# Optimization experiments

Hardware: AMD Instinct MI355X
Metric: run time of the kernel (lower is better)

## Reference

```python
import jax, jax.numpy as jnp
import numpy as np

STRIDES = (8, 16, 32, 64, 128)
IMG = 1024
RANGES = ((-1.0, 64.0), (64.0, 128.0), (128.0, 256.0), (256.0, 512.0), (512.0, 1e8))
NUM_CLASSES = 15
TOPK = 15
BG_LABEL = 15  # hardcoded in the torch source
G = 32


def _grid():
    pts, rr, spp = [], [], []
    for s, (lo, hi) in zip(STRIDES, RANGES):
        n = IMG // s
        ys, xs = np.meshgrid(np.arange(n), np.arange(n), indexing='ij')
        p = np.stack([xs.ravel() * s + s / 2.0, ys.ravel() * s + s / 2.0], axis=-1)
        pts.append(p)
        rr.append(np.tile(np.array([lo, hi]), (n * n, 1)))
        spp.append(np.full(n * n, s, np.float32))
    return (np.concatenate(pts).astype(np.float32),
            np.concatenate(rr).astype(np.float32),
            np.concatenate(spp).astype(np.float32))


def setup_inputs():
    key = jax.random.key(0)
    k = jax.random.split(key, 7)
    pts, rr, spp = _grid()
    N = pts.shape[0]
    ctr = jax.random.uniform(k[0], (G, 2), minval=64.0, maxval=IMG - 64.0)
    wh = jax.random.uniform(k[1], (G, 2), minval=16.0, maxval=256.0)
    ang = jax.random.uniform(k[2], (G, 1), minval=-jnp.pi / 2, maxval=jnp.pi / 2)
    gt_bboxes = jnp.concatenate([ctr, wh, ang], -1)
    gt_labels = jax.random.randint(k[3], (G,), 0, NUM_CLASSES)
    dist = jax.random.uniform(k[4], (N, 4), minval=0.1, maxval=8.0)
    angp = jax.random.normal(k[5], (N, 1)) * 0.3
    bbox_preds = jnp.concatenate([dist, angp], -1)
    probs = jax.random.normal(k[6], (N, NUM_CLASSES))
    return {"points": jnp.asarray(pts), "regress_ranges": jnp.asarray(rr),
            "stride_pp": jnp.asarray(spp), "gt_bboxes": gt_bboxes,
            "gt_labels": gt_labels, "bbox_preds": bbox_preds, "probs": probs}


def _cross(a, b):
    return a[..., 0] * b[..., 1] - a[..., 1] * b[..., 0]


def _corners(boxes):
    # [...,5] (cx,cy,w,h,a) -> [...,4,2]
    c, s = jnp.cos(boxes[..., 4]), jnp.sin(boxes[..., 4])
    w2, h2 = boxes[..., 2] / 2, boxes[..., 3] / 2
    dx = jnp.stack([w2, w2, -w2, -w2], -1)
    dy = jnp.stack([-h2, h2, h2, -h2], -1)
    x = boxes[..., 0:1] + dx * c[..., None] - dy * s[..., None]
    y = boxes[..., 1:2] + dx * s[..., None] + dy * c[..., None]
    return jnp.stack([x, y], -1)


def _in_obb(pts, boxes, eps=1e-6):
    r = pts - boxes[..., :2]
    c, s = jnp.cos(boxes[..., 4]), jnp.sin(boxes[..., 4])
    x = r[..., 0] * c + r[..., 1] * s
    y = -r[..., 0] * s + r[..., 1] * c
    return (jnp.abs(x) <= boxes[..., 2] / 2 + eps) & (jnp.abs(y) <= boxes[..., 3] / 2 + eps)


def pairwise_riou(b1, b2):
    # exact rotated-box IoU, b1 [N,5] x b2 [G,5] -> [N,G]
    N, Gn = b1.shape[0], b2.shape[0]
    c1, c2 = _corners(b1), _corners(b2)
    p = c1[:, None, :, None, :]
    d1 = (jnp.roll(c1, -1, 1) - c1)[:, None, :, None, :]
    q = c2[None, :, None, :, :]
    d2 = (jnp.roll(c2, -1, 1) - c2)[None, :, None, :, :]
    den = _cross(d1, d2)                     # [N,G,4,4]
    safe = jnp.where(jnp.abs(den) > 1e-10, den, 1.0)
    qp = q - p
    t = _cross(qp, d2) / safe
    u = _cross(qp, d1) / safe
    ok = (jnp.abs(den) > 1e-10) & (t >= 0) & (t <= 1) & (u >= 0) & (u <= 1)
    inter_pts = p + t[..., None] * d1        # [N,G,4,4,2]
    pts_a = inter_pts.reshape(N, Gn, 16, 2)
    ok_a = ok.reshape(N, Gn, 16)
    v1 = jnp.broadcast_to(c1[:, None], (N, Gn, 4, 2))
    ok1 = _in_obb(c1[:, None, :, :], b2[None, :, None, :])
    v2 = jnp.broadcast_to(c2[None, :], (N, Gn, 4, 2))
    ok2 = _in_obb(c2[None, :, :, :], b1[:, None, None, :])
    pts = jnp.concatenate([pts_a, v1, v2], 2)    # [N,G,24,2]
    okm = jnp.concatenate([ok_a, ok1, ok2], 2)
    cnt = okm.sum(-1)
    ctr = jnp.sum(pts * okm[..., None], 2) / jnp.maximum(cnt, 1)[..., None]
    pts = jnp.where(okm[..., None], pts, ctr[..., None, :])
    ang = jnp.where(okm, jnp.arctan2(pts[..., 1] - ctr[..., None, 1],
                                     pts[..., 0] - ctr[..., None, 0]), 1e9)
    order = jnp.argsort(ang, -1)
    pts_s = jnp.take_along_axis(pts, order[..., None], 2)
    m = jnp.maximum(cnt, 1)[..., None]
    nxt = (jnp.arange(24) + 1)[None, None] % m   # triangle-fan wrap over valid pts
    pts_n = jnp.take_along_axis(pts_s, nxt[..., None], 2)
    va = pts_s - ctr[..., None, :]
    vb = pts_n - ctr[..., None, :]
    inter = 0.5 * jnp.abs(jnp.sum(_cross(va, vb), -1))
    a1 = (b1[:, 2] * b1[:, 3])[:, None]
    a2 = (b2[:, 2] * b2[:, 3])[None]
    return inter / jnp.maximum(a1 + a2 - inter, 1e-8)


def _decode(points, preds):
    # DistanceAnglePointCoder.decode (le90)
    dist, angle = preds[:, :4], preds[:, 4]
    c, s = jnp.cos(angle), jnp.sin(angle)
    wh = dist[:, :2] + dist[:, 2:]
    ot = (dist[:, 2:] - dist[:, :2]) / 2
    ox = c * ot[:, 0] - s * ot[:, 1]
    oy = s * ot[:, 0] + c * ot[:, 1]
    ctr = points + jnp.stack([ox, oy], -1)
    a = (angle + jnp.pi / 2) % jnp.pi - jnp.pi / 2
    return jnp.concatenate([ctr, wh, a[:, None]], -1)


def _assign(points, regress_ranges, stride_pp, gt_bboxes, bbox_preds, probs, gt_labels):
    N = points.shape[0]
    Gn = gt_bboxes.shape[0]
    gt_ctr, gt_wh, gt_angle = gt_bboxes[:, :2], gt_bboxes[:, 2:4], gt_bboxes[:, 4]
    c, s = jnp.cos(gt_angle), jnp.sin(gt_angle)
    off = points[:, None, :] - gt_ctr[None]               # [N,G,2]
    ox = off[..., 0] * c + off[..., 1] * s                # rot_matrix [[c,s],[-s,c]] @ off
    oy = -off[..., 0] * s + off[..., 1] * c
    w, h = gt_wh[:, 0], gt_wh[:, 1]
    bbox_targets = jnp.stack([w / 2 + ox, h / 2 + oy, w / 2 - ox, h / 2 - oy], -1)  # l,t,r,b
    inside_gt = bbox_targets.min(-1) > 0
    centerness = jnp.maximum(1 - jnp.sqrt(((2 * ox / w) ** 2 + (2 * oy / h) ** 2 + 1e-8) / 2), 0.0)
    max_rd = bbox_targets.max(-1)
    inside_rr = (max_rd >= regress_ranges[:, None, 0]) & (max_rd <= regress_ranges[:, None, 1])
    ctr_r = 1.5 * stride_pp[:, None]
    inside_gt = inside_gt & (jnp.abs(ox) < ctr_r) & (jnp.abs(oy) < ctr_r)
    valid = inside_gt & inside_rr                          # [N,G]
    scaled = jnp.concatenate([bbox_preds[:, :4] * stride_pp[:, None], bbox_preds[:, 4:]], -1)
    det_rbboxes = _decode(points, scaled)
    iou = pairwise_riou(det_rbboxes, gt_bboxes)            # [N,G]
    det_probs = jax.nn.softmax(probs, -1)
    cost = (0.2 * centerness + 0.2 * iou + 0.6 * det_probs[:, gt_labels]) * valid
    vals, idxs = jax.lax.top_k(cost.T, TOPK)               # per-GT topk, [G,k]
    topk_mask = jnp.zeros((N, Gn), bool).at[idxs.T, jnp.arange(Gn)[None, :]].set(vals.T != 0)
    areas = (w * h)[None] * valid * topk_mask
    max_area = areas.max(1)
    inds = jnp.argmax(areas, 1)
    labels = jnp.where(max_area == 0, BG_LABEL, gt_labels[inds])
    # rematch GTs that got no candidate point (bincount logic)
    matched = (max_area != 0).astype(jnp.int32)
    counts = jnp.zeros(Gn, jnp.int32).at[inds].add(matched)
    anchor = jnp.argmax(centerness, 0)                     # best-centerness point per GT
    upd = jnp.where(counts == 0, anchor, N)                # N is OOB -> dropped
    inds = inds.at[upd].set(jnp.arange(Gn), mode='drop')
    labels = labels.at[upd].set(gt_labels, mode='drop')
    bt = jnp.take_along_axis(bbox_targets, inds[:, None, None], 1)[:, 0] / stride_pp[:, None]
    at = gt_angle[inds][:, None]
    return labels, bt, at


def reference(points, regress_ranges, stride_pp, gt_bboxes, gt_labels, bbox_preds, probs):
    return _assign(points, regress_ranges, stride_pp, gt_bboxes, bbox_preds, probs, gt_labels)
```

## Files before the change

kernel.cpp:

```cpp
#include <hip/hip_runtime.h>
#include <math.h>

#define NC 15
#define TOPKK 15
#define BG_F 15.0f
#define MAXC 256

__device__ __forceinline__ float obb_iou_reg(
    float cx1, float cy1, float w1, float h1, float a1,
    float cx2, float cy2, float w2, float h2, float a2) {
  const float dxs[4] = {0.5f, 0.5f, -0.5f, -0.5f};
  const float dys[4] = {-0.5f, 0.5f, 0.5f, -0.5f};
  float c1 = cosf(a1), s1 = sinf(a1), c2 = cosf(a2), s2 = sinf(a2);
  float ax[4], ay[4], bx[4], by[4];
#pragma unroll
  for (int k = 0; k < 4; k++) {
    float dx = dxs[k] * w1, dy = dys[k] * h1;
    ax[k] = cx1 + dx * c1 - dy * s1;
    ay[k] = cy1 + dx * s1 + dy * c1;
    dx = dxs[k] * w2; dy = dys[k] * h2;
    bx[k] = cx2 + dx * c2 - dy * s2;
    by[k] = cy2 + dx * s2 + dy * c2;
  }
  float qx[24], qy[24];
#pragma unroll
  for (int k = 0; k < 24; k++) { qx[k] = 0.f; qy[k] = 0.f; }
  unsigned valid = 0u;
#pragma unroll
  for (int e1 = 0; e1 < 4; e1++) {
    float d1x = ax[(e1 + 1) & 3] - ax[e1], d1y = ay[(e1 + 1) & 3] - ay[e1];
#pragma unroll
    for (int e2 = 0; e2 < 4; e2++) {
      float d2x = bx[(e2 + 1) & 3] - bx[e2], d2y = by[(e2 + 1) & 3] - by[e2];
      float den = d1x * d2y - d1y * d2x;
      float qpx = bx[e2] - ax[e1], qpy = by[e2] - ay[e1];
      float t = (qpx * d2y - qpy * d2x) / den;
      float u = (qpx * d1y - qpy * d1x) / den;
      bool ok = (fabsf(den) > 1e-10f) &&
                (t >= 0.f) && (t <= 1.f) && (u >= 0.f) && (u <= 1.f);
      if (ok) {
        qx[e1 * 4 + e2] = ax[e1] + t * d1x;
        qy[e1 * 4 + e2] = ay[e1] + t * d1y;
        valid |= (1u << (e1 * 4 + e2));
      }
    }
  }
  const float eps = 1e-6f;
#pragma unroll
  for (int k = 0; k < 4; k++) {
    float rx = ax[k] - cx2, ry = ay[k] - cy2;
    float x = rx * c2 + ry * s2, y = -rx * s2 + ry * c2;
    if (fabsf(x) <= w2 * 0.5f + eps && fabsf(y) <= h2 * 0.5f + eps) {
      qx[16 + k] = ax[k]; qy[16 + k] = ay[k];
      valid |= (1u << (16 + k));
    }
  }
#pragma unroll
  for (int k = 0; k < 4; k++) {
    float rx = bx[k] - cx1, ry = by[k] - cy1;
    float x = rx * c1 + ry * s1, y = -rx * s1 + ry * c1;
    if (fabsf(x) <= w1 * 0.5f + eps && fabsf(y) <= h1 * 0.5f + eps) {
      qx[20 + k] = bx[k]; qy[20 + k] = by[k];
      valid |= (1u << (20 + k));
    }
  }
  int cnt = __popc(valid);
  float inter = 0.f;
  if (cnt > 0) {
    float sx = 0.f, sy = 0.f;
#pragma unroll
    for (int k = 0; k < 24; k++) {
      bool v = (valid >> k) & 1u;
      sx += v ? qx[k] : 0.f;
      sy += v ? qy[k] : 0.f;
    }
    float ccx = sx / (float)cnt, ccy = sy / (float)cnt;
    float ang[24];
#pragma unroll
    for (int k = 0; k < 24; k++) {
      float a = atan2f(qy[k] - ccy, qx[k] - ccx);
      ang[k] = ((valid >> k) & 1u) ? a : 1e9f;
    }
    unsigned used = ~valid;
    float area2 = 0.f;
    float prevx = 0.f, prevy = 0.f, firstx = 0.f, firsty = 0.f;
    for (int s = 0; s < cnt; s++) {
      float ba = 1e30f, bxv = 0.f, byv = 0.f;
      int bk = 0;
#pragma unroll
      for (int k = 0; k < 24; k++) {
        bool avail = !((used >> k) & 1u);
        bool better = avail && (ang[k] < ba);
        if (better) { ba = ang[k]; bxv = qx[k]; byv = qy[k]; bk = k; }
      }
      used |= (1u << bk);
      float vx = bxv - ccx, vy = byv - ccy;
      if (s == 0) { firstx = vx; firsty = vy; }
      else { area2 += prevx * vy - prevy * vx; }
      prevx = vx; prevy = vy;
    }
    area2 += prevx * firsty - prevy * firstx;
    inter = 0.5f * fabsf(area2);
  }
  float areaA = w1 * h1, areaB = w2 * h2;
  return inter / fmaxf(areaA + areaB - inter, 1e-8f);
}

__global__ void k_scan(const float* __restrict__ pts,
                       const float* __restrict__ rr,
                       const float* __restrict__ spp,
                       const float* __restrict__ gtb,
                       int* __restrict__ cand_cnt,
                       int* __restrict__ cand_i,
                       unsigned long long* __restrict__ blk_cent,
                       unsigned long long* __restrict__ point_key,
                       int N, int G) {
  int blk = blockIdx.x;
  int g = blk % G, chunk = blk / G;
  int i = chunk * 256 + threadIdx.x;
  if (g == 0 && i < N) point_key[i] = 0ull;
  float gx = gtb[g * 5 + 0], gy = gtb[g * 5 + 1];
  float gw = gtb[g * 5 + 2], gh = gtb[g * 5 + 3], ga = gtb[g * 5 + 4];
  float cg = cosf(ga), sg = sinf(ga);
  float inv_gw = 2.f / gw, inv_gh = 2.f / gh;
  float hw = gw * 0.5f, hh = gh * 0.5f;

  unsigned long long key = 0ull;
  bool valid = false;
  if (i < N) {
    float2 p = ((const float2*)pts)[i];
    float px = p.x - gx, py = p.y - gy;
    float ox = px * cg + py * sg, oy = -px * sg + py * cg;
    float nx = ox * inv_gw, ny = oy * inv_gh;
    float ctn = fmaxf(1.f - sqrtf((nx * nx + ny * ny + 1e-8f) * 0.5f), 0.f);
    key = ((unsigned long long)__float_as_uint(ctn) << 32) |
          (unsigned long long)(0xFFFFFFFFu - (unsigned)i);
    float l = hw + ox, tt = hh + oy, r = hw - ox, b = hh - oy;
    float minb = fminf(fminf(l, tt), fminf(r, b));
    float maxb = fmaxf(fmaxf(l, tt), fmaxf(r, b));
    float cr = 1.5f * spp[i];
    float2 rv = ((const float2*)rr)[i];
    valid = (minb > 0.f) && (fabsf(ox) < cr) && (fabsf(oy) < cr) &&
            (maxb >= rv.x) && (maxb <= rv.y);
  }
  unsigned long long best = key;
#pragma unroll
  for (int o = 32; o > 0; o >>= 1) {
    unsigned long long other = __shfl_xor(best, o, 64);
    if (other > best) best = other;
  }
  __shared__ unsigned long long swin[4];
  int lane = threadIdx.x & 63, wid = threadIdx.x >> 6;
  if (lane == 0) swin[wid] = best;
  __syncthreads();
  if (threadIdx.x == 0) {
    unsigned long long m = swin[0];
#pragma unroll
    for (int q = 1; q < 4; q++) if (swin[q] > m) m = swin[q];
    blk_cent[blk] = m;
  }
  unsigned long long ball = __ballot(valid);
  if (ball) {
    int leader = __ffsll(ball) - 1;
    int base = 0;
    if (lane == leader) base = atomicAdd(&cand_cnt[g], __popcll(ball));
    base = __shfl(base, leader, 64);
    if (valid) {
      int slot = base + __popcll(ball & ((1ull << lane) - 1ull));
      if (slot < MAXC) cand_i[g * MAXC + slot] = i;
    }
  }
}

__global__ void k_all(const float* __restrict__ pts,
                      const float* __restrict__ spp,
                      const float* __restrict__ gtb,
                      const int* __restrict__ gtl,
                      const float* __restrict__ preds,
                      const float* __restrict__ probs,
                      const int* __restrict__ cand_cnt,
                      const int* __restrict__ cand_i,
                      const unsigned long long* __restrict__ blk_cent,
                      unsigned long long* __restrict__ cent_key,
                      unsigned long long* __restrict__ point_key,
                      int G, int CH) {
  int g = blockIdx.x;
  int tid = threadIdx.x;
  int lane = tid & 63, wid = tid >> 6;
  float gx = gtb[g * 5 + 0], gy = gtb[g * 5 + 1];
  float gw = gtb[g * 5 + 2], gh = gtb[g * 5 + 3], ga = gtb[g * 5 + 4];
  float cg = cosf(ga), sg = sinf(ga);
  float inv_gw = 2.f / gw, inv_gh = 2.f / gh;
  __shared__ unsigned long long swin[4];

  unsigned long long best = 0ull;
  for (int c = tid; c < CH; c += 256) {
    unsigned long long e = blk_cent[(size_t)c * G + g];
    if (e > best) best = e;
  }
#pragma unroll
  for (int o = 32; o > 0; o >>= 1) {
    unsigned long long other = __shfl_xor(best, o, 64);
    if (other > best) best = other;
  }
  if (lane == 0) swin[wid] = best;
  __syncthreads();
  if (tid == 0) {
    unsigned long long m = swin[0];
#pragma unroll
    for (int q = 1; q < 4; q++) if (swin[q] > m) m = swin[q];
    cent_key[g] = m;
  }
  __syncthreads();

  int cnt = cand_cnt[g];
  if (cnt > MAXC) cnt = MAXC;

  unsigned long long key = 0ull;
  if (tid < cnt) {
    int i = cand_i[g * MAXC + tid];
    float ptx = pts[i * 2 + 0], pty = pts[i * 2 + 1];
    float px = ptx - gx, py = pty - gy;
    float ox = px * cg + py * sg, oy = -px * sg + py * cg;
    float nx = ox * inv_gw, ny = oy * inv_gh;
    float ctn = fmaxf(1.f - sqrtf((nx * nx + ny * ny + 1e-8f) * 0.5f), 0.f);

    float pv[NC];
    float m = -1e30f;
#pragma unroll
    for (int k = 0; k < NC; k++) { pv[k] = probs[i * NC + k]; m = fmaxf(m, pv[k]); }
    float ss = 0.f;
#pragma unroll
    for (int k = 0; k < NC; k++) { pv[k] = expf(pv[k] - m); ss += pv[k]; }
    float prob = pv[gtl[g]] / ss;

    float st = spp[i];
    float d0 = preds[i * 5 + 0] * st, d1 = preds[i * 5 + 1] * st;
    float d2 = preds[i * 5 + 2] * st, d3 = preds[i * 5 + 3] * st;
    float angp = preds[i * 5 + 4];
    float c = cosf(angp), s = sinf(angp);
    float w = d0 + d2, h = d1 + d3;
    float otx = (d2 - d0) * 0.5f, oty = (d3 - d1) * 0.5f;
    float dox = c * otx - s * oty, doy = s * otx + c * oty;
    const float PI = 3.14159265358979323846f;
    float a = fmodf(angp + PI * 0.5f, PI);
    if (a < 0.f) a += PI;
    a -= PI * 0.5f;

    float iou = obb_iou_reg(ptx + dox, pty + doy, w, h, a,
                            gx, gy, gw, gh, ga);
    float cval = 0.2f * ctn + 0.2f * iou + 0.6f * prob;
    key = ((unsigned long long)__float_as_uint(cval) << 32) |
          (unsigned long long)(0xFFFFFFFFu - (unsigned)i);
  }

  float area = gw * gh;
  unsigned long long area_key =
      (((unsigned long long)__float_as_uint(area)) << 32) |
      (unsigned long long)(unsigned)(G - 1 - g);
  int rounds = cnt < TOPKK ? cnt : TOPKK;
  for (int r = 0; r < rounds; r++) {
    unsigned long long k2 = key;
#pragma unroll
    for (int o = 32; o > 0; o >>= 1) {
      unsigned long long other = __shfl_xor(k2, o, 64);
      if (other > k2) k2 = other;
    }
    if (lane == 0) swin[wid] = k2;
    __syncthreads();
    unsigned long long w = swin[0];
#pragma unroll
    for (int q = 1; q < 4; q++) if (swin[q] > w) w = swin[q];
    __syncthreads();
    if (w == 0ull) break;
    if (key == w) key = 0ull;
    if (tid == 0) {
      unsigned iwin = 0xFFFFFFFFu - (unsigned)(w & 0xFFFFFFFFull);
      atomicMax(&point_key[iwin], area_key);
    }
  }
}

__global__ void k_assign(const unsigned long long* __restrict__ point_key,
                         const float* __restrict__ pts,
                         const float* __restrict__ spp,
                         const float* __restrict__ gtb,
                         const int* __restrict__ gtl,
                         int* __restrict__ counts,
                         float* __restrict__ out_labels,
                         float* __restrict__ out_bt,
                         float* __restrict__ out_at,
                         int N, int G) {
  int i = blockIdx.x * blockDim.x + threadIdx.x;
  if (i >= N) return;
  unsigned long long key = point_key[i];
  int g = 0;
  if (key != 0ull) {
    g = (G - 1) - (int)(key & 0xFFFFFFFFull);
    out_labels[i] = (float)gtl[g];
    atomicAdd(&counts[g], 1);
  } else {
    out_labels[i] = BG_F;
  }
  float gx = gtb[g * 5 + 0], gy = gtb[g * 5 + 1];
  float gw = gtb[g * 5 + 2], gh = gtb[g * 5 + 3], ga = gtb[g * 5 + 4];
  float cg = cosf(ga), sg = sinf(ga);
  float px = pts[i * 2 + 0] - gx, py = pts[i * 2 + 1] - gy;
  float ox = px * cg + py * sg, oy = -px * sg + py * cg;
  float st = spp[i];
  out_bt[i * 4 + 0] = (gw * 0.5f + ox) / st;
  out_bt[i * 4 + 1] = (gh * 0.5f + oy) / st;
  out_bt[i * 4 + 2] = (gw * 0.5f - ox) / st;
  out_bt[i * 4 + 3] = (gh * 0.5f - oy) / st;
  out_at[i] = ga;
}

__global__ void k_fix(const int* __restrict__ counts,
                      const unsigned long long* __restrict__ cent_key,
                      const float* __restrict__ pts,
                      const float* __restrict__ spp,
                      const float* __restrict__ gtb,
                      const int* __restrict__ gtl,
                      float* __restrict__ out_labels,
                      float* __restrict__ out_bt,
                      float* __restrict__ out_at,
                      int G) {
  int g = threadIdx.x;
  bool active = (g < G) && (counts[g] == 0);
  unsigned anchor = 0xFFFFFFFFu;
  if (active) anchor = 0xFFFFFFFFu - (unsigned)(cent_key[g] & 0xFFFFFFFFull);
  unsigned long long act = __ballot(active);
  bool winner = active;
  for (int o = 0; o < 64; o++) {
    unsigned oa = __shfl(anchor, o, 64);
    if (active && o > g && ((act >> o) & 1ull) && oa == anchor) winner = false;
  }
  if (winner) {
    unsigned i = anchor;
    out_labels[i] = (float)gtl[g];
    float gx = gtb[g * 5 + 0], gy = gtb[g * 5 + 1];
    float gw = gtb[g * 5 + 2], gh = gtb[g * 5 + 3], ga = gtb[g * 5 + 4];
    float cg = cosf(ga), sg = sinf(ga);
    float px = pts[i * 2 + 0] - gx, py = pts[i * 2 + 1] - gy;
    float ox = px * cg + py * sg, oy = -px * sg + py * cg;
    float st = spp[i];
    out_bt[i * 4 + 0] = (gw * 0.5f + ox) / st;
    out_bt[i * 4 + 1] = (gh * 0.5f + oy) / st;
    out_bt[i * 4 + 2] = (gw * 0.5f - ox) / st;
    out_bt[i * 4 + 3] = (gh * 0.5f - oy) / st;
    out_at[i] = ga;
  }
}

extern "C" void kernel_launch(void* const* d_in, const int* in_sizes, int n_in,
                              void* d_out, int out_size, void* d_ws, size_t ws_size,
                              hipStream_t stream) {
  const float* pts   = (const float*)d_in[0];
  const float* rr    = (const float*)d_in[1];
  const float* spp   = (const float*)d_in[2];
  const float* gtb   = (const float*)d_in[3];
  const int*   gtl   = (const int*)d_in[4];
  const float* preds = (const float*)d_in[5];
  const float* probs = (const float*)d_in[6];
  int N = in_sizes[0] / 2;
  int G = in_sizes[3] / 5;
  int CH = (N + 255) / 256;

  float* out = (float*)d_out;
  float* out_labels = out;
  float* out_bt     = out + N;
  float* out_at     = out + 5 * (size_t)N;

  int* cand_cnt = (int*)d_ws;
  int* counts   = cand_cnt + G;
  unsigned long long* cent_key  = (unsigned long long*)(counts + G);
  unsigned long long* point_key = cent_key + G;
  unsigned long long* blk_cent  = point_key + N;
  int* cand_i = (int*)(blk_cent + (size_t)CH * G);

  hipMemsetAsync(d_ws, 0, (size_t)G * 8, stream);

  const int thr = 256;
  hipLaunchKernelGGL(k_scan, dim3(CH * G), dim3(thr), 0, stream,
                     pts, rr, spp, gtb, cand_cnt, cand_i,
                     blk_cent, point_key, N, G);
  hipLaunchKernelGGL(k_all, dim3(G), dim3(thr), 0, stream,
                     pts, spp, gtb, gtl, preds, probs,
                     cand_cnt, cand_i, blk_cent, cent_key, point_key, G, CH);
  hipLaunchKernelGGL(k_assign, dim3((N + thr - 1) / thr), dim3(thr), 0, stream,
                     point_key, pts, spp, gtb, gtl, counts,
                     out_labels, out_bt, out_at, N, G);
  hipLaunchKernelGGL(k_fix, dim3(1), dim3(64), 0, stream,
                     counts, cent_key, pts, spp, gtb, gtl,
                     out_labels, out_bt, out_at, G);
}
```

Measured before the change: 103.2 us.

## Split candidate scoring into wide kernel, use block-level atomics and padded counters

The per-GT candidate scoring (softmax, rotated IoU) moves out of the single-block-per-GT kernel into a new kernel that launches four 64-thread blocks per GT, so the heavy work spreads over more CUs. A separate top-k kernel then reads the precomputed keys. The scan kernel now takes one atomic per block instead of one per wave, and the per-GT counters are padded to 32-int strides to avoid contention on shared cache lines. The cost is one extra kernel launch and a round trip of the candidate keys through global memory.

New measurement: 105.0 us. About the same (+1.7%).

```diff
diff --git a/kernel.cpp b/kernel.cpp
--- a/kernel.cpp
+++ b/kernel.cpp
@@ -5,6 +5,7 @@
 #define TOPKK 15
 #define BG_F 15.0f
 #define MAXC 256
+#define CSTRIDE 32
 
 __device__ __forceinline__ float obb_iou_reg(
     float cx1, float cy1, float w1, float h1, float a1,
@@ -143,6 +144,7 @@
     valid = (minb > 0.f) && (fabsf(ox) < cr) && (fabsf(oy) < cr) &&
             (maxb >= rv.x) && (maxb <= rv.y);
   }
+  int lane = threadIdx.x & 63, wid = threadIdx.x >> 6;
   unsigned long long best = key;
 #pragma unroll
   for (int o = 32; o > 0; o >>= 1) {
@@ -150,36 +152,89 @@
     if (other > best) best = other;
   }
   __shared__ unsigned long long swin[4];
-  int lane = threadIdx.x & 63, wid = threadIdx.x >> 6;
-  if (lane == 0) swin[wid] = best;
+  __shared__ int s_wcnt[4];
+  __shared__ int s_base;
+  unsigned long long ball = __ballot(valid);
+  if (lane == 0) {
+    swin[wid] = best;
+    s_wcnt[wid] = __popcll(ball);
+  }
   __syncthreads();
   if (threadIdx.x == 0) {
     unsigned long long m = swin[0];
 #pragma unroll
     for (int q = 1; q < 4; q++) if (swin[q] > m) m = swin[q];
     blk_cent[blk] = m;
-  }
-  unsigned long long ball = __ballot(valid);
-  if (ball) {
-    int leader = __ffsll(ball) - 1;
-    int base = 0;
-    if (lane == leader) base = atomicAdd(&cand_cnt[g], __popcll(ball));
-    base = __shfl(base, leader, 64);
-    if (valid) {
-      int slot = base + __popcll(ball & ((1ull << lane) - 1ull));
-      if (slot < MAXC) cand_i[g * MAXC + slot] = i;
-    }
-  }
-}
-
-__global__ void k_all(const float* __restrict__ pts,
-                      const float* __restrict__ spp,
-                      const float* __restrict__ gtb,
-                      const int* __restrict__ gtl,
-                      const float* __restrict__ preds,
-                      const float* __restrict__ probs,
+    int tot = s_wcnt[0] + s_wcnt[1] + s_wcnt[2] + s_wcnt[3];
+    s_base = (tot > 0) ? atomicAdd(&cand_cnt[g * CSTRIDE], tot) : 0;
+  }
+  __syncthreads();
+  if (valid) {
+    int woff = 0;
+    for (int q = 0; q < wid; q++) woff += s_wcnt[q];
+    int slot = s_base + woff + __popcll(ball & ((1ull << lane) - 1ull));
+    if (slot < MAXC) cand_i[g * MAXC + slot] = i;
+  }
+}
+
+__global__ void k_heavy(const float* __restrict__ pts,
+                        const float* __restrict__ spp,
+                        const float* __restrict__ gtb,
+                        const int* __restrict__ gtl,
+                        const float* __restrict__ preds,
+                        const float* __restrict__ probs,
+                        const int* __restrict__ cand_cnt,
+                        const int* __restrict__ cand_i,
+                        unsigned long long* __restrict__ cand_key,
+                        int G) {
+  int b = blockIdx.x;
+  int g = b >> 2, q = b & 3;
+  int slot = q * 64 + threadIdx.x;
+  int cnt = cand_cnt[g * CSTRIDE];
+  if (cnt > MAXC) cnt = MAXC;
+  if (slot >= cnt) return;
+  int i = cand_i[g * MAXC + slot];
+  float gx = gtb[g * 5 + 0], gy = gtb[g * 5 + 1];
+  float gw = gtb[g * 5 + 2], gh = gtb[g * 5 + 3], ga = gtb[g * 5 + 4];
+  float cg = cosf(ga), sg = sinf(ga);
+  float ptx = pts[i * 2 + 0], pty = pts[i * 2 + 1];
+  float px = ptx - gx, py = pty - gy;
+  float ox = px * cg + py * sg, oy = -px * sg + py * cg;
+  float nx = 2.f * ox / gw, ny = 2.f * oy / gh;
+  float ctn = fmaxf(1.f - sqrtf((nx * nx + ny * ny + 1e-8f) * 0.5f), 0.f);
+
+  float pv[NC];
+  float m = -1e30f;
+#pragma unroll
+  for (int k = 0; k < NC; k++) { pv[k] = probs[i * NC + k]; m = fmaxf(m, pv[k]); }
+  float ss = 0.f;
+#pragma unroll
+  for (int k = 0; k < NC; k++) { pv[k] = expf(pv[k] - m); ss += pv[k]; }
+  float prob = pv[gtl[g]] / ss;
+
+  float st = spp[i];
+  float d0 = preds[i * 5 + 0] * st, d1 = preds[i * 5 + 1] * st;
+  float d2 = preds[i * 5 + 2] * st, d3 = preds[i * 5 + 3] * st;
+  float angp = preds[i * 5 + 4];
+  float c = cosf(angp), s = sinf(angp);
+  float w = d0 + d2, h = d1 + d3;
+  float otx = (d2 - d0) * 0.5f, oty = (d3 - d1) * 0.5f;
+  float dox = c * otx - s * oty, doy = s * otx + c * oty;
+  const float PI = 3.14159265358979323846f;
+  float a = fmodf(angp + PI * 0.5f, PI);
+  if (a < 0.f) a += PI;
+  a -= PI * 0.5f;
+
+  float iou = obb_iou_reg(ptx + dox, pty + doy, w, h, a, gx, gy, gw, gh, ga);
+  float cval = 0.2f * ctn + 0.2f * iou + 0.6f * prob;
+  cand_key[g * MAXC + slot] =
+      ((unsigned long long)__float_as_uint(cval) << 32) |
+      (unsigned long long)(0xFFFFFFFFu - (unsigned)i);
+}
+
+__global__ void k_top(const float* __restrict__ gtb,
                       const int* __restrict__ cand_cnt,
-                      const int* __restrict__ cand_i,
+                      const unsigned long long* __restrict__ cand_key,
                       const unsigned long long* __restrict__ blk_cent,
                       unsigned long long* __restrict__ cent_key,
                       unsigned long long* __restrict__ point_key,
@@ -187,10 +242,6 @@
   int g = blockIdx.x;
   int tid = threadIdx.x;
   int lane = tid & 63, wid = tid >> 6;
-  float gx = gtb[g * 5 + 0], gy = gtb[g * 5 + 1];
-  float gw = gtb[g * 5 + 2], gh = gtb[g * 5 + 3], ga = gtb[g * 5 + 4];
-  float cg = cosf(ga), sg = sinf(ga);
-  float inv_gw = 2.f / gw, inv_gh = 2.f / gh;
   __shared__ unsigned long long swin[4];
 
   unsigned long long best = 0ull;
@@ -213,48 +264,11 @@
   }
   __syncthreads();
 
-  int cnt = cand_cnt[g];
+  int cnt = cand_cnt[g * CSTRIDE];
   if (cnt > MAXC) cnt = MAXC;
-
-  unsigned long long key = 0ull;
-  if (tid < cnt) {
-    int i = cand_i[g * MAXC + tid];
-    float ptx = pts[i * 2 + 0], pty = pts[i * 2 + 1];
-    float px = ptx - gx, py = pty - gy;
-    float ox = px * cg + py * sg, oy = -px * sg + py * cg;
-    float nx = ox * inv_gw, ny = oy * inv_gh;
-    float ctn = fmaxf(1.f - sqrtf((nx * nx + ny * ny + 1e-8f) * 0.5f), 0.f);
-
-    float pv[NC];
-    float m = -1e30f;
-#pragma unroll
-    for (int k = 0; k < NC; k++) { pv[k] = probs[i * NC + k]; m = fmaxf(m, pv[k]); }
-    float ss = 0.f;
-#pragma unroll
-    for (int k = 0; k < NC; k++) { pv[k] = expf(pv[k] - m); ss += pv[k]; }
-    float prob = pv[gtl[g]] / ss;
-
-    float st = spp[i];
-    float d0 = preds[i * 5 + 0] * st, d1 = preds[i * 5 + 1] * st;
-    float d2 = preds[i * 5 + 2] * st, d3 = preds[i * 5 + 3] * st;
-    float angp = preds[i * 5 + 4];
-    float c = cosf(angp), s = sinf(angp);
-    float w = d0 + d2, h = d1 + d3;
-    float otx = (d2 - d0) * 0.5f, oty = (d3 - d1) * 0.5f;
-    float dox = c * otx - s * oty, doy = s * otx + c * oty;
-    const float PI = 3.14159265358979323846f;
-    float a = fmodf(angp + PI * 0.5f, PI);
-    if (a < 0.f) a += PI;
-    a -= PI * 0.5f;
-
-    float iou = obb_iou_reg(ptx + dox, pty + doy, w, h, a,
-                            gx, gy, gw, gh, ga);
-    float cval = 0.2f * ctn + 0.2f * iou + 0.6f * prob;
-    key = ((unsigned long long)__float_as_uint(cval) << 32) |
-          (unsigned long long)(0xFFFFFFFFu - (unsigned)i);
-  }
-
-  float area = gw * gh;
+  unsigned long long key = (tid < cnt) ? cand_key[g * MAXC + tid] : 0ull;
+
+  float area = gtb[g * 5 + 2] * gtb[g * 5 + 3];
   unsigned long long area_key =
       (((unsigned long long)__float_as_uint(area)) << 32) |
       (unsigned long long)(unsigned)(G - 1 - g);
@@ -298,7 +312,7 @@
   if (key != 0ull) {
     g = (G - 1) - (int)(key & 0xFFFFFFFFull);
     out_labels[i] = (float)gtl[g];
-    atomicAdd(&counts[g], 1);
+    atomicAdd(&counts[g * CSTRIDE], 1);
   } else {
     out_labels[i] = BG_F;
   }
@@ -326,7 +340,7 @@
                       float* __restrict__ out_at,
                       int G) {
   int g = threadIdx.x;
-  bool active = (g < G) && (counts[g] == 0);
+  bool active = (g < G) && (counts[g * CSTRIDE] == 0);
   unsigned anchor = 0xFFFFFFFFu;
   if (active) anchor = 0xFFFFFFFFu - (unsigned)(cent_key[g] & 0xFFFFFFFFull);
   unsigned long long act = __ballot(active);
@@ -372,21 +386,27 @@
   float* out_at     = out + 5 * (size_t)N;
 
   int* cand_cnt = (int*)d_ws;
-  int* counts   = cand_cnt + G;
-  unsigned long long* cent_key  = (unsigned long long*)(counts + G);
+  int* counts   = cand_cnt + G * CSTRIDE;
+  unsigned long long* cent_key =
+      (unsigned long long*)(counts + G * CSTRIDE);
   unsigned long long* point_key = cent_key + G;
   unsigned long long* blk_cent  = point_key + N;
   int* cand_i = (int*)(blk_cent + (size_t)CH * G);
-
-  hipMemsetAsync(d_ws, 0, (size_t)G * 8, stream);
+  unsigned long long* cand_key =
+      (unsigned long long*)(cand_i + (size_t)G * MAXC);
+
+  hipMemsetAsync(d_ws, 0, (size_t)G * CSTRIDE * 4 * 2, stream);
 
   const int thr = 256;
   hipLaunchKernelGGL(k_scan, dim3(CH * G), dim3(thr), 0, stream,
                      pts, rr, spp, gtb, cand_cnt, cand_i,
                      blk_cent, point_key, N, G);
-  hipLaunchKernelGGL(k_all, dim3(G), dim3(thr), 0, stream,
+  hipLaunchKernelGGL(k_heavy, dim3(G * 4), dim3(64), 0, stream,
                      pts, spp, gtb, gtl, preds, probs,
-                     cand_cnt, cand_i, blk_cent, cent_key, point_key, G, CH);
+                     cand_cnt, cand_i, cand_key, G);
+  hipLaunchKernelGGL(k_top, dim3(G), dim3(thr), 0, stream,
+                     gtb, cand_cnt, cand_key, blk_cent,
+                     cent_key, point_key, G, CH);
   hipLaunchKernelGGL(k_assign, dim3((N + thr - 1) / thr), dim3(thr), 0, stream,
                      point_key, pts, spp, gtb, gtl, counts,
                      out_labels, out_bt, out_at, N, G);
```

## Fold memset and fix-up kernel into neighbours; replace atomic candidate compaction with per-block lists

Applied to the files above, without the earlier changes.

The scan kernel no longer does a global atomicAdd per wavefront to append candidates. Each block instead writes its own capped candidate list and count, and the per-GT kernel gathers them through a shared-memory prefix scan. The workspace memset goes away because counters are now zeroed inside k_all. The separate k_fix launch is folded into k_assign using a last-block-done atomic counter with fences. Together this cuts two stream operations and removes atomic contention, at the cost of a serial prefix scan, padded counters, and a per-block candidate cap of 32 that would truncate if a block ever held more valid points.

New measurement: 105.2 us. Within noise of the previous version (+1.9%).

```diff
diff --git a/kernel.cpp b/kernel.cpp
--- a/kernel.cpp
+++ b/kernel.cpp
@@ -5,6 +5,8 @@
 #define TOPKK 15
 #define BG_F 15.0f
 #define MAXC 256
+#define CAP 32
+#define CSTRIDE 32
 
 __device__ __forceinline__ float obb_iou_reg(
     float cx1, float cy1, float w1, float h1, float a1,
@@ -110,8 +112,8 @@
                        const float* __restrict__ rr,
                        const float* __restrict__ spp,
                        const float* __restrict__ gtb,
-                       int* __restrict__ cand_cnt,
-                       int* __restrict__ cand_i,
+                       int* __restrict__ blk_cnt,
+                       int* __restrict__ blk_ci,
                        unsigned long long* __restrict__ blk_cent,
                        unsigned long long* __restrict__ point_key,
                        int N, int G) {
@@ -143,6 +145,7 @@
     valid = (minb > 0.f) && (fabsf(ox) < cr) && (fabsf(oy) < cr) &&
             (maxb >= rv.x) && (maxb <= rv.y);
   }
+  int lane = threadIdx.x & 63, wid = threadIdx.x >> 6;
   unsigned long long best = key;
 #pragma unroll
   for (int o = 32; o > 0; o >>= 1) {
@@ -150,25 +153,26 @@
     if (other > best) best = other;
   }
   __shared__ unsigned long long swin[4];
-  int lane = threadIdx.x & 63, wid = threadIdx.x >> 6;
-  if (lane == 0) swin[wid] = best;
+  __shared__ int s_wcnt[4];
+  unsigned long long ball = __ballot(valid);
+  if (lane == 0) {
+    swin[wid] = best;
+    s_wcnt[wid] = __popcll(ball);
+  }
   __syncthreads();
   if (threadIdx.x == 0) {
     unsigned long long m = swin[0];
 #pragma unroll
     for (int q = 1; q < 4; q++) if (swin[q] > m) m = swin[q];
     blk_cent[blk] = m;
-  }
-  unsigned long long ball = __ballot(valid);
-  if (ball) {
-    int leader = __ffsll(ball) - 1;
-    int base = 0;
-    if (lane == leader) base = atomicAdd(&cand_cnt[g], __popcll(ball));
-    base = __shfl(base, leader, 64);
-    if (valid) {
-      int slot = base + __popcll(ball & ((1ull << lane) - 1ull));
-      if (slot < MAXC) cand_i[g * MAXC + slot] = i;
-    }
+    int tot = s_wcnt[0] + s_wcnt[1] + s_wcnt[2] + s_wcnt[3];
+    blk_cnt[blk] = (tot < CAP) ? tot : CAP;
+  }
+  if (valid) {
+    int woff = 0;
+    for (int q = 0; q < wid; q++) woff += s_wcnt[q];
+    int slot = woff + __popcll(ball & ((1ull << lane) - 1ull));
+    if (slot < CAP) blk_ci[blk * CAP + slot] = i;
   }
 }
 
@@ -178,47 +182,62 @@
                       const int* __restrict__ gtl,
                       const float* __restrict__ preds,
                       const float* __restrict__ probs,
-                      const int* __restrict__ cand_cnt,
-                      const int* __restrict__ cand_i,
+                      const int* __restrict__ blk_cnt,
+                      const int* __restrict__ blk_ci,
                       const unsigned long long* __restrict__ blk_cent,
                       unsigned long long* __restrict__ cent_key,
                       unsigned long long* __restrict__ point_key,
+                      int* __restrict__ counts,
+                      int* __restrict__ done,
                       int G, int CH) {
   int g = blockIdx.x;
   int tid = threadIdx.x;
   int lane = tid & 63, wid = tid >> 6;
+  __shared__ unsigned long long swin[4];
+  __shared__ int s_pre[129];
+
+  if (tid == 0) counts[g * CSTRIDE] = 0;
+  if (g == 0 && tid == 0) *done = 0;
+
+  unsigned long long best = 0ull;
+  for (int c = tid; c < CH; c += 256) {
+    unsigned long long e = blk_cent[(size_t)c * G + g];
+    if (e > best) best = e;
+  }
+#pragma unroll
+  for (int o = 32; o > 0; o >>= 1) {
+    unsigned long long other = __shfl_xor(best, o, 64);
+    if (other > best) best = other;
+  }
+  if (lane == 0) swin[wid] = best;
+  __syncthreads();
+  if (tid == 0) {
+    unsigned long long m = swin[0];
+#pragma unroll
+    for (int q = 1; q < 4; q++) if (swin[q] > m) m = swin[q];
+    cent_key[g] = m;
+  }
+
+  if (tid < CH) s_pre[tid + 1] = blk_cnt[tid * G + g];
+  __syncthreads();
+  if (tid == 0) {
+    s_pre[0] = 0;
+    for (int c = 1; c <= CH; c++) s_pre[c] += s_pre[c - 1];
+  }
+  __syncthreads();
+  int cnt = s_pre[CH];
+  if (cnt > MAXC) cnt = MAXC;
+
   float gx = gtb[g * 5 + 0], gy = gtb[g * 5 + 1];
   float gw = gtb[g * 5 + 2], gh = gtb[g * 5 + 3], ga = gtb[g * 5 + 4];
   float cg = cosf(ga), sg = sinf(ga);
   float inv_gw = 2.f / gw, inv_gh = 2.f / gh;
-  __shared__ unsigned long long swin[4];
-
-  unsigned long long best = 0ull;
-  for (int c = tid; c < CH; c += 256) {
-    unsigned long long e = blk_cent[(size_t)c * G + g];
-    if (e > best) best = e;
-  }
-#pragma unroll
-  for (int o = 32; o > 0; o >>= 1) {
-    unsigned long long other = __shfl_xor(best, o, 64);
-    if (other > best) best = other;
-  }
-  if (lane == 0) swin[wid] = best;
-  __syncthreads();
-  if (tid == 0) {
-    unsigned long long m = swin[0];
-#pragma unroll
-    for (int q = 1; q < 4; q++) if (swin[q] > m) m = swin[q];
-    cent_key[g] = m;
-  }
-  __syncthreads();
-
-  int cnt = cand_cnt[g];
-  if (cnt > MAXC) cnt = MAXC;
 
   unsigned long long key = 0ull;
   if (tid < cnt) {
-    int i = cand_i[g * MAXC + tid];
+    int c = 0;
+    while (s_pre[c + 1] <= tid) c++;
+    int i = blk_ci[((size_t)c * G + g) * CAP + (tid - s_pre[c])];
     float ptx = pts[i * 2 + 0], pty = pts[i * 2 + 1];
     float px = ptx - gx, py = pty - gy;
     float ox = px * cg + py * sg, oy = -px * sg + py * cg;
@@ -238,10 +257,10 @@
     float d0 = preds[i * 5 + 0] * st, d1 = preds[i * 5 + 1] * st;
     float d2 = preds[i * 5 + 2] * st, d3 = preds[i * 5 + 3] * st;
     float angp = preds[i * 5 + 4];
-    float c = cosf(angp), s = sinf(angp);
+    float c2 = cosf(angp), s2 = sinf(angp);
     float w = d0 + d2, h = d1 + d3;
     float otx = (d2 - d0) * 0.5f, oty = (d3 - d1) * 0.5f;
-    float dox = c * otx - s * oty, doy = s * otx + c * oty;
+    float dox = c2 * otx - s2 * oty, doy = s2 * otx + c2 * oty;
     const float PI = 3.14159265358979323846f;
     float a = fmodf(angp + PI * 0.5f, PI);
     if (a < 0.f) a += PI;
@@ -286,58 +305,24 @@
                          const float* __restrict__ spp,
                          const float* __restrict__ gtb,
                          const int* __restrict__ gtl,
+                         const unsigned long long* __restrict__ cent_key,
                          int* __restrict__ counts,
+                         int* __restrict__ done,
                          float* __restrict__ out_labels,
                          float* __restrict__ out_bt,
                          float* __restrict__ out_at,
                          int N, int G) {
   int i = blockIdx.x * blockDim.x + threadIdx.x;
-  if (i >= N) return;
-  unsigned long long key = point_key[i];
-  int g = 0;
-  if (key != 0ull) {
-    g = (G - 1) - (int)(key & 0xFFFFFFFFull);
-    out_labels[i] = (float)gtl[g];
-    atomicAdd(&counts[g], 1);
-  } else {
-    out_labels[i] = BG_F;
-  }
-  float gx = gtb[g * 5 + 0], gy = gtb[g * 5 + 1];
-  float gw = gtb[g * 5 + 2], gh = gtb[g * 5 + 3], ga = gtb[g * 5 + 4];
-  float cg = cosf(ga), sg = sinf(ga);
-  float px = pts[i * 2 + 0] - gx, py = pts[i * 2 + 1] - gy;
-  float ox = px * cg + py * sg, oy = -px * sg + py * cg;
-  float st = spp[i];
-  out_bt[i * 4 + 0] = (gw * 0.5f + ox) / st;
-  out_bt[i * 4 + 1] = (gh * 0.5f + oy) / st;
-  out_bt[i * 4 + 2] = (gw * 0.5f - ox) / st;
-  out_bt[i * 4 + 3] = (gh * 0.5f - oy) / st;
-  out_at[i] = ga;
-}
-
-__global__ void k_fix(const int* __restrict__ counts,
-                      const unsigned long long* __restrict__ cent_key,
-                      const float* __restrict__ pts,
-                      const float* __restrict__ spp,
-                      const float* __restrict__ gtb,
-                      const int* __restrict__ gtl,
-                      float* __restrict__ out_labels,
-                      float* __restrict__ out_bt,
-                      float* __restrict__ out_at,
-                      int G) {
-  int g = threadIdx.x;
-  bool active = (g < G) && (counts[g] == 0);
-  unsigned anchor = 0xFFFFFFFFu;
-  if (active) anchor = 0xFFFFFFFFu - (unsigned)(cent_key[g] & 0xFFFFFFFFull);
-  unsigned long long act = __ballot(active);
-  bool winner = active;
-  for (int o = 0; o < 64; o++) {
-    unsigned oa = __shfl(anchor, o, 64);
-    if (active && o > g && ((act >> o) & 1ull) && oa == anchor) winner = false;
-  }
-  if (winner) {
-    unsigned i = anchor;
-    out_labels[i] = (float)gtl[g];
+  if (i < N) {
+    unsigned long long key = point_key[i];
+    int g = 0;
+    if (key != 0ull) {
+      g = (G - 1) - (int)(key & 0xFFFFFFFFull);
+      out_labels[i] = (float)gtl[g];
+      atomicAdd(&counts[g * CSTRIDE], 1);
+    } else {
+      out_labels[i] = BG_F;
+    }
     float gx = gtb[g * 5 + 0], gy = gtb[g * 5 + 1];
     float gw = gtb[g * 5 + 2], gh = gtb[g * 5 + 3], ga = gtb[g * 5 + 4];
     float cg = cosf(ga), sg = sinf(ga);
@@ -349,6 +334,42 @@
     out_bt[i * 4 + 2] = (gw * 0.5f - ox) / st;
     out_bt[i * 4 + 3] = (gh * 0.5f - oy) / st;
     out_at[i] = ga;
+  }
+  __shared__ int s_old;
+  __syncthreads();
+  if (threadIdx.x == 0) {
+    __threadfence();
+    s_old = atomicAdd(done, 1);
+  }
+  __syncthreads();
+  if (s_old == (int)gridDim.x - 1 && threadIdx.x < 64) {
+    __threadfence();
+    int g = threadIdx.x;
+    bool active = false;
+    if (g < G) active = (atomicAdd(&counts[g * CSTRIDE], 0) == 0);
+    unsigned anchor = 0xFFFFFFFFu;
+    if (active) anchor = 0xFFFFFFFFu - (unsigned)(cent_key[g] & 0xFFFFFFFFull);
+    unsigned long long act = __ballot(active);
+    bool winner = active;
+    for (int o = 0; o < 64; o++) {
+      unsigned oa = __shfl(anchor, o, 64);
+      if (active && o > g && ((act >> o) & 1ull) && oa == anchor) winner = false;
+    }
+    if (winner) {
+      unsigned i2 = anchor;
+      out_labels[i2] = (float)gtl[g];
+      float gx = gtb[g * 5 + 0], gy = gtb[g * 5 + 1];
+      float gw = gtb[g * 5 + 2], gh = gtb[g * 5 + 3], ga = gtb[g * 5 + 4];
+      float cg = cosf(ga), sg = sinf(ga);
+      float px = pts[i2 * 2 + 0] - gx, py = pts[i2 * 2 + 1] - gy;
+      float ox = px * cg + py * sg, oy = -px * sg + py * cg;
+      float st = spp[i2];
+      out_bt[i2 * 4 + 0] = (gw * 0.5f + ox) / st;
+      out_bt[i2 * 4 + 1] = (gh * 0.5f + oy) / st;
+      out_bt[i2 * 4 + 2] = (gw * 0.5f - ox) / st;
+      out_bt[i2 * 4 + 3] = (gh * 0.5f - oy) / st;
+      out_at[i2] = ga;
+    }
   }
 }
 
@@ -371,26 +392,24 @@
   float* out_bt     = out + N;
   float* out_at     = out + 5 * (size_t)N;
 
-  int* cand_cnt = (int*)d_ws;
-  int* counts   = cand_cnt + G;
-  unsigned long long* cent_key  = (unsigned long long*)(counts + G);
+  int* counts = (int*)d_ws;
+  int* done   = counts + G * CSTRIDE;
+  unsigned long long* cent_key =
+      (unsigned long long*)(done + CSTRIDE);
   unsigned long long* point_key = cent_key + G;
   unsigned long long* blk_cent  = point_key + N;
-  int* cand_i = (int*)(blk_cent + (size_t)CH * G);
-
-  hipMemsetAsync(d_ws, 0, (size_t)G * 8, stream);
+  int* blk_cnt = (int*)(blk_cent + (size_t)CH * G);
+  int* blk_ci  = blk_cnt + (size_t)CH * G;
 
   const int thr = 256;
   hipLaunchKernelGGL(k_scan, dim3(CH * G), dim3(thr), 0, stream,
-                     pts, rr, spp, gtb, cand_cnt, cand_i,
+                     pts, rr, spp, gtb, blk_cnt, blk_ci,
                      blk_cent, point_key, N, G);
   hipLaunchKernelGGL(k_all, dim3(G), dim3(thr), 0, stream,
                      pts, spp, gtb, gtl, preds, probs,
-                     cand_cnt, cand_i, blk_cent, cent_key, point_key, G, CH);
+                     blk_cnt, blk_ci, blk_cent, cent_key, point_key,
+                     counts, done, G, CH);
   hipLaunchKernelGGL(k_assign, dim3((N + thr - 1) / thr), dim3(thr), 0, stream,
-                     point_key, pts, spp, gtb, gtl, counts,
-                     out_labels, out_bt, out_at, N, G);
-  hipLaunchKernelGGL(k_fix, dim3(1), dim3(64), 0, stream,
-                     counts, cent_key, pts, spp, gtb, gtl,
-                     out_labels, out_bt, out_at, G);
+                     point_key, pts, spp, gtb, gtl, cent_key,
+                     counts, done, out_labels, out_bt, out_at, N, G);
 }
```
